# Optimization experiments

Hardware: AMD Instinct MI355X
Metric: run time of the kernel (lower is better)

Reference implementation:

```python
import jax, jax.numpy as jnp
import numpy as np

COST_CLASS, COST_BBOX, COST_GIOU = 1.0, 5.0, 2.0
NUM_FRAMES, Q_PER_FRAME, NUM_TGT, NUM_CLASSES = 36, 100, 20, 92
B = 64


def box_cxcywh_to_xyxy(b):
    cx, cy, w, h = b[..., 0], b[..., 1], b[..., 2], b[..., 3]
    return jnp.stack([cx - 0.5 * w, cy - 0.5 * h, cx + 0.5 * w, cy + 0.5 * h], axis=-1)


def pairwise_giou(b1, b2):
    # b1: [..., Q, 4], b2: [..., T, 4], xyxy -> giou [..., Q, T]
    area1 = (b1[..., 2] - b1[..., 0]) * (b1[..., 3] - b1[..., 1])
    area2 = (b2[..., 2] - b2[..., 0]) * (b2[..., 3] - b2[..., 1])
    lt = jnp.maximum(b1[..., :, None, :2], b2[..., None, :, :2])
    rb = jnp.minimum(b1[..., :, None, 2:], b2[..., None, :, 2:])
    wh = jnp.clip(rb - lt, 0.0)
    inter = wh[..., 0] * wh[..., 1]
    union = area1[..., :, None] + area2[..., None, :] - inter
    iou = inter / union
    lt_e = jnp.minimum(b1[..., :, None, :2], b2[..., None, :, :2])
    rb_e = jnp.maximum(b1[..., :, None, 2:], b2[..., None, :, 2:])
    wh_e = jnp.clip(rb_e - lt_e, 0.0)
    area_e = wh_e[..., 0] * wh_e[..., 1]
    return iou - (area_e - union) / area_e


def compute_cost(pred_logits, pred_boxes, tgt_labels, tgt_boxes):
    b = pred_logits.shape[0]
    prob = jax.nn.softmax(pred_logits.reshape(b, NUM_FRAMES, Q_PER_FRAME, -1), axis=-1)  # [B,F,Q,C]
    pb = pred_boxes.reshape(b, NUM_FRAMES, Q_PER_FRAME, 4)
    lab = jnp.transpose(tgt_labels, (1, 0, 2))            # [B,F,T]
    tb = jnp.transpose(tgt_boxes, (1, 0, 2, 3))           # [B,F,T,4]
    onehot = jax.nn.one_hot(lab, prob.shape[-1], dtype=prob.dtype)  # [B,F,T,C]
    cost_class = -jnp.einsum('bfqc,bftc->bfqt', prob, onehot)
    cost_bbox = jnp.abs(pb[:, :, :, None, :] - tb[:, :, None, :, :]).sum(-1)  # L1 cdist
    giou = pairwise_giou(box_cxcywh_to_xyxy(pb), box_cxcywh_to_xyxy(tb))
    return COST_CLASS * cost_class + COST_BBOX * cost_bbox - COST_GIOU * giou


def auction_assign(cost):
    # cost [Q, T]; returns obj_of [T]: query index assigned to each target.
    # eps-optimal auction algorithm (replaces scipy linear_sum_assignment).
    Q, T = cost.shape
    benefit = -cost.T  # [T, Q]
    spread = jnp.max(benefit) - jnp.min(benefit) + 1e-6
    eps = spread / 1000.0
    neg_inf = jnp.asarray(-1e30, cost.dtype)

    def cond(s):
        _, _, obj_of, it = s
        return jnp.logical_and(jnp.any(obj_of < 0), it < 20000)

    def body(s):
        price, owner, obj_of, it = s
        unassigned = obj_of < 0                       # [T]
        vals = benefit - price[None, :]               # [T, Q]
        top2v, top2i = jax.lax.top_k(vals, 2)
        best_obj = top2i[:, 0]                        # [T]
        bid = price[best_obj] + (top2v[:, 0] - top2v[:, 1]) + eps
        bid = jnp.where(unassigned, bid, neg_inf)
        best_bid = jnp.full((Q,), neg_inf, cost.dtype).at[best_obj].max(bid)
        pids = jnp.arange(T, dtype=jnp.int32)
        win = unassigned & (bid >= best_bid[best_obj])
        winner = jnp.full((Q,), T, jnp.int32).at[best_obj].min(jnp.where(win, pids, T))
        has_bid = winner < T
        # evict previous owners of objects that received a bid
        evict = jnp.where(has_bid & (owner >= 0), owner, T)
        obj_of = obj_of.at[evict].set(-1, mode='drop')
        qids = jnp.arange(Q, dtype=jnp.int32)
        obj_of = obj_of.at[jnp.where(has_bid, winner, T)].set(jnp.where(has_bid, qids, -1), mode='drop')
        price = jnp.where(has_bid, best_bid, price)
        owner = jnp.where(has_bid, winner, owner)
        return price, owner, obj_of, it + 1

    init = (jnp.zeros((Q,), cost.dtype), jnp.full((Q,), -1, jnp.int32),
            jnp.full((T,), -1, jnp.int32), jnp.int32(0))
    _, _, obj_of, _ = jax.lax.while_loop(cond, body, init)
    return obj_of


def setup_inputs() -> dict:
    key = jax.random.key(0)
    k1, k2, k3, k4 = jax.random.split(key, 4)
    pred_logits = jax.random.normal(k1, (B, NUM_FRAMES * Q_PER_FRAME, NUM_CLASSES), jnp.float32)
    pred_boxes = jax.random.uniform(k2, (B, NUM_FRAMES * Q_PER_FRAME, 4), jnp.float32)
    tgt_labels = jax.random.randint(k3, (NUM_FRAMES, B, NUM_TGT), 0, NUM_CLASSES, jnp.int32)
    tgt_boxes = jax.random.uniform(k4, (NUM_FRAMES, B, NUM_TGT, 4), jnp.float32)
    return {'pred_logits': pred_logits, 'pred_boxes': pred_boxes,
            'tgt_labels': tgt_labels, 'tgt_boxes': tgt_boxes}


def reference(pred_logits, pred_boxes, tgt_labels, tgt_boxes):
    cost = compute_cost(pred_logits, pred_boxes, tgt_labels, tgt_boxes)  # [B,F,Q,T]
    b, f, q, t = cost.shape
    obj_of = jax.vmap(auction_assign)(cost.reshape(b * f, q, t))  # [BF, T]
    order = jnp.argsort(obj_of, axis=-1)  # scipy returns rows ascending
    pred_idx = jnp.take_along_axis(obj_of, order, axis=-1).reshape(b, f, t)
    tgt_idx = order.astype(jnp.int32).reshape(b, f, t)
    return cost, pred_idx, tgt_idx
```

## Files before the change

kernel.cpp:

```cpp
#include <hip/hip_runtime.h>

#define NF 36
#define QN 100
#define TN 20
#define CN 92
#define NB 64
#define BSTR 104

__global__ __launch_bounds__(64) void matcher_kernel(
    const float* __restrict__ logits,
    const float* __restrict__ pboxes,
    const int*   __restrict__ tlabels,
    const float* __restrict__ tboxes,
    float* __restrict__ out_cost,
    float* __restrict__ out_pred,
    float* __restrict__ out_tgt)
{
    const int bf = blockIdx.x;
    const int b  = bf / NF;
    const int f  = bf % NF;
    const int lane = threadIdx.x;

    __shared__ float ben[TN][BSTR];
    __shared__ float price[BSTR];
    __shared__ int   owner[QN];
    __shared__ float bidv[TN];
    __shared__ int   bo[TN];
    __shared__ int   evict[TN];
    __shared__ int   objl[TN];
    __shared__ int   slab[TN];
    __shared__ float tbr[TN][4];
    __shared__ float tbx[TN][4];
    __shared__ float tarea[TN];

    if (lane < TN) {
        const int base = (f * NB + b) * TN + lane;
        slab[lane] = tlabels[base];
        const float* tb = tboxes + (size_t)base * 4;
        float cx = tb[0], cy = tb[1], w = tb[2], h = tb[3];
        tbr[lane][0] = cx; tbr[lane][1] = cy; tbr[lane][2] = w; tbr[lane][3] = h;
        float x1 = cx - 0.5f * w, y1 = cy - 0.5f * h;
        float x2 = cx + 0.5f * w, y2 = cy + 0.5f * h;
        tbx[lane][0] = x1; tbx[lane][1] = y1; tbx[lane][2] = x2; tbx[lane][3] = y2;
        tarea[lane] = (x2 - x1) * (y2 - y1);
        evict[lane] = 0;
    }
    __syncthreads();

    float mn = INFINITY, mx = -INFINITY;
    for (int p = 0; p < 2; ++p) {
        const int q = lane + 64 * p;
        if (q < QN) {
            const size_t row = (size_t)b * (NF * QN) + (size_t)f * QN + q;
            const float* L = logits + row * CN;
            const float4* L4 = reinterpret_cast<const float4*>(L);
            float4 r[23];
            #pragma unroll
            for (int i = 0; i < 23; ++i) r[i] = L4[i];
            float m = -INFINITY;
            #pragma unroll
            for (int i = 0; i < 23; ++i) {
                float4 v = r[i];
                m = fmaxf(m, v.x); m = fmaxf(m, v.y); m = fmaxf(m, v.z); m = fmaxf(m, v.w);
            }
            float s = 0.f;
            #pragma unroll
            for (int i = 0; i < 23; ++i) {
                float4 v = r[i];
                s += expf(v.x - m); s += expf(v.y - m); s += expf(v.z - m); s += expf(v.w - m);
            }

            float4 pbv = reinterpret_cast<const float4*>(pboxes)[row];
            float cx = pbv.x, cy = pbv.y, w = pbv.z, h = pbv.w;
            float px1 = cx - 0.5f * w, py1 = cy - 0.5f * h;
            float px2 = cx + 0.5f * w, py2 = cy + 0.5f * h;
            float a1 = (px2 - px1) * (py2 - py1);

            for (int t = 0; t < TN; ++t) {
                float pc = expf(L[slab[t]] - m) / s;
                float cb = fabsf(cx - tbr[t][0]) + fabsf(cy - tbr[t][1]);
                cb = cb + fabsf(w - tbr[t][2]);
                cb = cb + fabsf(h - tbr[t][3]);
                float ltx = fmaxf(px1, tbx[t][0]), lty = fmaxf(py1, tbx[t][1]);
                float rbx = fminf(px2, tbx[t][2]), rby = fminf(py2, tbx[t][3]);
                float wx = fmaxf(rbx - ltx, 0.f), wy = fmaxf(rby - lty, 0.f);
                float inter = wx * wy;
                float uni = a1 + tarea[t] - inter;
                float iou = inter / uni;
                float ex1 = fminf(px1, tbx[t][0]), ey1 = fminf(py1, tbx[t][1]);
                float ex2 = fmaxf(px2, tbx[t][2]), ey2 = fmaxf(py2, tbx[t][3]);
                float ew = fmaxf(ex2 - ex1, 0.f), eh = fmaxf(ey2 - ey1, 0.f);
                float ae = ew * eh;
                float giou = iou - (ae - uni) / ae;
                float cost = (-pc) + 5.0f * cb - 2.0f * giou;
                ben[t][q] = -cost;
                mn = fminf(mn, cost);
                mx = fmaxf(mx, cost);
            }
        }
    }

    for (int i = lane; i < BSTR; i += 64) price[i] = 0.f;
    for (int i = lane; i < QN; i += 64) owner[i] = -1;
    if (lane < TN) {
        ben[lane][100] = -INFINITY; ben[lane][101] = -INFINITY;
        ben[lane][102] = -INFINITY; ben[lane][103] = -INFINITY;
    }
    __syncthreads();

    #pragma unroll
    for (int off = 32; off > 0; off >>= 1) {
        mn = fminf(mn, __shfl_xor(mn, off, 64));
        mx = fmaxf(mx, __shfl_xor(mx, off, 64));
    }
    const float eps = (((-mn) - (-mx)) + 1e-6f) / 1000.0f;

    {
        float4* dst = reinterpret_cast<float4*>(out_cost + (size_t)bf * (QN * TN));
        for (int i = lane; i < (QN * TN) / 4; i += 64) {
            int k = i * 4;
            int q = k / TN, t0 = k - q * TN;
            float4 v;
            v.x = -ben[t0 + 0][q]; v.y = -ben[t0 + 1][q];
            v.z = -ben[t0 + 2][q]; v.w = -ben[t0 + 3][q];
            dst[i] = v;
        }
    }

    const int myt = lane / 3;
    const int jj  = lane - myt * 3;
    const int q0  = jj * 34;
    const bool is_leader = (lane < 60) && (jj == 0);
    float breg[34];
    {
        const int tt = (lane < 60) ? myt : 0;
        #pragma unroll
        for (int k = 0; k < 34; ++k) breg[k] = ben[tt][q0 + k];
    }
    int myobj = -1;

    for (int it = 0; it < 20000; ++it) {
        unsigned long long U = __ballot(is_leader && (myobj < 0));
        if (U == 0ull) break;

        float v0 = -INFINITY, v1 = -INFINITY; int i0 = q0;
        #pragma unroll
        for (int k = 0; k < 34; ++k) {
            float v = breg[k] - price[q0 + k];
            bool c = v > v0;
            v1 = c ? v0 : fmaxf(v1, v);
            i0 = c ? (q0 + k) : i0;
            v0 = c ? v : v0;
        }
        {
            float av0 = __shfl_down(v0, 1), av1 = __shfl_down(v1, 1);
            int   ai0 = __shfl_down(i0, 1);
            float bv0 = __shfl_down(v0, 2), bv1 = __shfl_down(v1, 2);
            int   bi0 = __shfl_down(i0, 2);
            if (av0 > v0) { v1 = fmaxf(v0, av1); v0 = av0; i0 = ai0; }
            else          { v1 = fmaxf(av0, v1); }
            if (bv0 > v0) { v1 = fmaxf(v0, bv1); v0 = bv0; i0 = bi0; }
            else          { v1 = fmaxf(bv0, v1); }
        }
        float mybid = price[i0] + (v0 - v1) + eps;
        if (is_leader) { bidv[myt] = mybid; bo[myt] = i0; }
        __syncthreads();

        const bool act = is_leader && (((U >> lane) & 1ull) != 0ull);
        if (act) {
            bool lose = false;
            unsigned long long u = U;
            while (u) {
                int pos = __builtin_ctzll(u); u &= (u - 1);
                int t2 = pos / 3;
                if (t2 != myt) {
                    float bv = bidv[t2]; int ob = bo[t2];
                    lose = lose || (ob == i0 && (bv > mybid || (bv == mybid && t2 < myt)));
                }
            }
            if (!lose) {
                int q = i0;
                int old = owner[q];
                owner[q] = myt;
                price[q] = mybid;
                myobj = q;
                if (old >= 0) evict[old] = 1;
            }
        }
        __syncthreads();
        if (is_leader && evict[myt]) { myobj = -1; evict[myt] = 0; }
    }
    __syncthreads();
    if (is_leader) objl[myt] = myobj;
    __syncthreads();

    if (lane < TN) {
        int v = objl[lane];
        int r = 0;
        for (int u = 0; u < TN; ++u) {
            int w = objl[u];
            r += (w < v) || (w == v && u < lane);
        }
        out_pred[(size_t)bf * TN + r] = (float)v;
        out_tgt[(size_t)bf * TN + r]  = (float)lane;
    }
}

extern "C" void kernel_launch(void* const* d_in, const int* in_sizes, int n_in,
                              void* d_out, int out_size, void* d_ws, size_t ws_size,
                              hipStream_t stream) {
    const float* logits  = (const float*)d_in[0];
    const float* pboxes  = (const float*)d_in[1];
    const int*   tlabels = (const int*)d_in[2];
    const float* tboxes  = (const float*)d_in[3];

    float* out = (float*)d_out;
    float* out_cost = out;
    float* out_pred = out + (size_t)NB * NF * QN * TN;
    float* out_tgt  = out_pred + (size_t)NB * NF * TN;

    hipLaunchKernelGGL(matcher_kernel, dim3(NB * NF), dim3(64), 0, stream,
                       logits, pboxes, tlabels, tboxes, out_cost, out_pred, out_tgt);
}
```

Baseline: 180.6 us.

## Resolve auction bids via wave shuffles, drop owner/evict tables and a barrier

Bid conflict resolution and eviction move from shared-memory arrays to wavefront shuffles, which removes the owner/evict/bid tables and one __syncthreads per auction iteration. A single-bidder fast path skips the full 20-way shuffle scan. Benefit rows are loaded as float4 and split across three lanes with three independent running-argmax chains, and the winning price is carried along so the dependent price reload goes away. The shuffle scan adds ALU work for each iteration with several bidders, and eviction detection now depends on all lanes seeing consistent state within the wave.

New measurement: 185.9 us. +2.9%, slower.

```diff
diff --git a/kernel.cpp b/kernel.cpp
--- a/kernel.cpp
+++ b/kernel.cpp
@@ -6,6 +6,8 @@
 #define CN 92
 #define NB 64
 #define BSTR 104
+
+struct T2 { float v0, v1, p0; int i0; };
 
 __global__ __launch_bounds__(64) void matcher_kernel(
     const float* __restrict__ logits,
@@ -21,12 +23,8 @@
     const int f  = bf % NF;
     const int lane = threadIdx.x;
 
-    __shared__ float ben[TN][BSTR];
-    __shared__ float price[BSTR];
-    __shared__ int   owner[QN];
-    __shared__ float bidv[TN];
-    __shared__ int   bo[TN];
-    __shared__ int   evict[TN];
+    __shared__ __align__(16) float ben[TN][BSTR];
+    __shared__ __align__(16) float price[BSTR];
     __shared__ int   objl[TN];
     __shared__ int   slab[TN];
     __shared__ float tbr[TN][4];
@@ -43,7 +41,6 @@
         float x2 = cx + 0.5f * w, y2 = cy + 0.5f * h;
         tbx[lane][0] = x1; tbx[lane][1] = y1; tbx[lane][2] = x2; tbx[lane][3] = y2;
         tarea[lane] = (x2 - x1) * (y2 - y1);
-        evict[lane] = 0;
     }
     __syncthreads();
 
@@ -101,7 +98,6 @@
     }
 
     for (int i = lane; i < BSTR; i += 64) price[i] = 0.f;
-    for (int i = lane; i < QN; i += 64) owner[i] = -1;
     if (lane < TN) {
         ben[lane][100] = -INFINITY; ben[lane][101] = -INFINITY;
         ben[lane][102] = -INFINITY; ben[lane][103] = -INFINITY;
@@ -129,66 +125,71 @@
 
     const int myt = lane / 3;
     const int jj  = lane - myt * 3;
-    const int q0  = jj * 34;
+    const int q0  = (jj == 0) ? 0 : (jj == 1 ? 36 : 68);
     const bool is_leader = (lane < 60) && (jj == 0);
-    float breg[34];
+    float4 br[9];
     {
         const int tt = (lane < 60) ? myt : 0;
+        const float4* rp = reinterpret_cast<const float4*>(&ben[tt][q0]);
         #pragma unroll
-        for (int k = 0; k < 34; ++k) breg[k] = ben[tt][q0 + k];
+        for (int k = 0; k < 9; ++k) br[k] = rp[k];
     }
     int myobj = -1;
 
+    auto step4 = [&](T2& X, int fi) {
+        float4 pv = *reinterpret_cast<const float4*>(&price[q0 + 4 * fi]);
+        float4 bv = br[fi];
+        { float v = bv.x - pv.x; bool c = v > X.v0; X.v1 = c ? X.v0 : fmaxf(X.v1, v); X.i0 = c ? (q0+4*fi+0) : X.i0; X.p0 = c ? pv.x : X.p0; X.v0 = c ? v : X.v0; }
+        { float v = bv.y - pv.y; bool c = v > X.v0; X.v1 = c ? X.v0 : fmaxf(X.v1, v); X.i0 = c ? (q0+4*fi+1) : X.i0; X.p0 = c ? pv.y : X.p0; X.v0 = c ? v : X.v0; }
+        { float v = bv.z - pv.z; bool c = v > X.v0; X.v1 = c ? X.v0 : fmaxf(X.v1, v); X.i0 = c ? (q0+4*fi+2) : X.i0; X.p0 = c ? pv.z : X.p0; X.v0 = c ? v : X.v0; }
+        { float v = bv.w - pv.w; bool c = v > X.v0; X.v1 = c ? X.v0 : fmaxf(X.v1, v); X.i0 = c ? (q0+4*fi+3) : X.i0; X.p0 = c ? pv.w : X.p0; X.v0 = c ? v : X.v0; }
+    };
+    auto mergeT = [&](T2& L, const T2& R) {
+        if (R.v0 > L.v0) { L.v1 = fmaxf(L.v0, R.v1); L.v0 = R.v0; L.i0 = R.i0; L.p0 = R.p0; }
+        else             { L.v1 = fmaxf(R.v0, L.v1); }
+    };
+
     for (int it = 0; it < 20000; ++it) {
-        unsigned long long U = __ballot(is_leader && (myobj < 0));
+        const bool active = is_leader && (myobj < 0);
+        unsigned long long U = __ballot(active);
         if (U == 0ull) break;
 
-        float v0 = -INFINITY, v1 = -INFINITY; int i0 = q0;
-        #pragma unroll
-        for (int k = 0; k < 34; ++k) {
-            float v = breg[k] - price[q0 + k];
-            bool c = v > v0;
-            v1 = c ? v0 : fmaxf(v1, v);
-            i0 = c ? (q0 + k) : i0;
-            v0 = c ? v : v0;
-        }
+        T2 A{-INFINITY, -INFINITY, 0.f, q0};
+        T2 Bc{-INFINITY, -INFINITY, 0.f, q0 + 12};
+        T2 Cc{-INFINITY, -INFINITY, 0.f, q0 + 24};
+        step4(A, 0);  step4(A, 1);  step4(A, 2);
+        step4(Bc, 3); step4(Bc, 4); step4(Bc, 5);
+        step4(Cc, 6); step4(Cc, 7);
+        if (jj != 1) step4(Cc, 8);
+        mergeT(A, Bc); mergeT(A, Cc);
+
         {
-            float av0 = __shfl_down(v0, 1), av1 = __shfl_down(v1, 1);
-            int   ai0 = __shfl_down(i0, 1);
-            float bv0 = __shfl_down(v0, 2), bv1 = __shfl_down(v1, 2);
-            int   bi0 = __shfl_down(i0, 2);
-            if (av0 > v0) { v1 = fmaxf(v0, av1); v0 = av0; i0 = ai0; }
-            else          { v1 = fmaxf(av0, v1); }
-            if (bv0 > v0) { v1 = fmaxf(v0, bv1); v0 = bv0; i0 = bi0; }
-            else          { v1 = fmaxf(bv0, v1); }
-        }
-        float mybid = price[i0] + (v0 - v1) + eps;
-        if (is_leader) { bidv[myt] = mybid; bo[myt] = i0; }
+            T2 R1{__shfl_down(A.v0, 1), __shfl_down(A.v1, 1), __shfl_down(A.p0, 1), __shfl_down(A.i0, 1)};
+            T2 R2{__shfl_down(A.v0, 2), __shfl_down(A.v1, 2), __shfl_down(A.p0, 2), __shfl_down(A.i0, 2)};
+            mergeT(A, R1); mergeT(A, R2);
+        }
+        float mybid = A.p0 + (A.v0 - A.v1) + eps;
+        float bb_ = active ? mybid : -INFINITY;
+        int   bq  = A.i0;
+
+        bool lose = false, evicted = false;
+        if (__popcll(U) == 1) {
+            int src = (int)__builtin_ctzll(U);
+            int sq = __shfl(bq, src);
+            evicted = (myobj == sq);
+        } else {
+            #pragma unroll
+            for (int t2 = 0; t2 < TN; ++t2) {
+                float sb = __shfl(bb_, 3 * t2);
+                int   sq = __shfl(bq, 3 * t2);
+                bool a2 = (sb != -INFINITY);
+                lose    = lose    || (a2 && sq == bq   && (sb > bb_ || (sb == bb_ && t2 < myt)));
+                evicted = evicted || (a2 && sq == myobj);
+            }
+        }
+        if (active && !lose) { price[bq] = mybid; myobj = bq; }
+        else if (is_leader && evicted && myobj >= 0) myobj = -1;
         __syncthreads();
-
-        const bool act = is_leader && (((U >> lane) & 1ull) != 0ull);
-        if (act) {
-            bool lose = false;
-            unsigned long long u = U;
-            while (u) {
-                int pos = __builtin_ctzll(u); u &= (u - 1);
-                int t2 = pos / 3;
-                if (t2 != myt) {
-                    float bv = bidv[t2]; int ob = bo[t2];
-                    lose = lose || (ob == i0 && (bv > mybid || (bv == mybid && t2 < myt)));
-                }
-            }
-            if (!lose) {
-                int q = i0;
-                int old = owner[q];
-                owner[q] = myt;
-                price[q] = mybid;
-                myobj = q;
-                if (old >= 0) evict[old] = 1;
-            }
-        }
-        __syncthreads();
-        if (is_leader && evict[myt]) { myobj = -1; evict[myt] = 0; }
     }
     __syncthreads();
     if (is_leader) objl[myt] = myobj;
```
